# Kernel optimization log

Hardware: AMD Instinct MI355X
Metric: run time of the kernel (lower is better)

The kernel has to match this reference:

```python
import jax, jax.numpy as jnp
import numpy as np

STRIDE = 10  # matches init_kwargs

def setup_inputs() -> dict:
    key = jax.random.key(0)
    x = jax.random.normal(key, (64, 1000, 128), dtype=jnp.float32)
    return {"x": x}

def reference(x):
    B, T, F = x.shape
    L = T // STRIDE  # number of windows
    # (B, L, S, F): non-overlapping windows of length STRIDE
    xr = x.reshape(B, L, STRIDE, F)
    mean = xr.mean(axis=2, keepdims=True)          # avg_pool(ksize=stride, strides=stride)
    ms = xr - mean                                  # means_subtracted
    std = jnp.sqrt(jnp.mean(ms * ms, axis=2))       # (B, L, F), population std
    # per-window covariance: (B, L, F, F)
    cov = jnp.einsum('blsk,blsm->blkm', ms, ms) / STRIDE
    # strictly-lower-triangle indices, row-major order == tf.boolean_mask order
    i, j = np.tril_indices(F, -1)
    cov_v = cov[..., i, j]                          # (B, L, F*(F-1)/2)
    den_v = std[..., i] * std[..., j]               # gather std pairs directly
    safe = jnp.where(den_v == 0, jnp.float32(1.0), den_v)
    return jnp.where(den_v == 0, jnp.float32(0.0), cov_v / safe)  # divide_no_nan
```

## Files before the change

### kernel.cpp

```cpp
#include <hip/hip_runtime.h>

#define BATCH 64
#define TLEN 1000
#define F 128
#define S 10
#define L 100
#define NPAIR 8128
#define NTILE 528
#define NT4 (NPAIR / 4)
#define BLOCK 512

__global__ __launch_bounds__(BLOCK, 8) void corr_kernel(const float* __restrict__ x,
                                                        float* __restrict__ out) {
    const int win = blockIdx.x;
    const int b = win / L;
    const int l = win % L;
    const int tid = threadIdx.x;

    __shared__ float ms[S][F];
    __shared__ __align__(16) float tri[NPAIR];

    const float4* src4 = (const float4*)(x + ((size_t)b * TLEN + (size_t)l * S) * F);
    if (tid < (S * F) / 4) ((float4*)&ms[0][0])[tid] = src4[tid];
    __syncthreads();

    if (tid < F) {
        const int f = tid;
        float col[S];
        float sum = 0.f;
        #pragma unroll
        for (int s = 0; s < S; ++s) { col[s] = ms[s][f]; sum += col[s]; }
        const float mean = sum * (1.0f / S);
        float sq = 0.f;
        #pragma unroll
        for (int s = 0; s < S; ++s) { float d = col[s] - mean; col[s] = d; sq += d * d; }
        const float stdv = sqrtf(sq * (1.0f / S));
        const float r = (stdv == 0.f) ? 0.f : 0.31622776601683794f / stdv;
        #pragma unroll
        for (int s = 0; s < S; ++s) ms[s][f] = col[s] * r;
    }
    __syncthreads();

    for (int t = tid; t < NTILE; t += BLOCK) {
        int ti = (int)((sqrtf(8.0f * (float)t + 1.0f) - 1.0f) * 0.5f);
        while ((ti + 1) * (ti + 2) / 2 <= t) ++ti;
        while (ti * (ti + 1) / 2 > t) --ti;
        const int tj = t - ti * (ti + 1) / 2;

        float acc[4][4];
        #pragma unroll
        for (int a = 0; a < 4; ++a)
            #pragma unroll
            for (int c = 0; c < 4; ++c) acc[a][c] = 0.f;

        #pragma unroll
        for (int s = 0; s < S; ++s) {
            const float4 av = *(const float4*)&ms[s][ti * 4];
            const float4 bv = *(const float4*)&ms[s][tj * 4];
            const float a0[4] = {av.x, av.y, av.z, av.w};
            const float b0[4] = {bv.x, bv.y, bv.z, bv.w};
            #pragma unroll
            for (int di = 0; di < 4; ++di)
                #pragma unroll
                for (int dj = 0; dj < 4; ++dj)
                    acc[di][dj] += a0[di] * b0[dj];
        }

        #pragma unroll
        for (int di = 0; di < 4; ++di) {
            const int i = ti * 4 + di;
            const int rowoff = i * (i - 1) / 2 + tj * 4;
            #pragma unroll
            for (int k = 0; k < 4; ++k) {
                const int dj = (k + tid) & 3;
                const int j = tj * 4 + dj;
                if (j < i) tri[rowoff + dj] = acc[di][dj];
            }
        }
    }
    __syncthreads();

    const float4* t4 = (const float4*)tri;
    float4* o4 = (float4*)(out + (size_t)win * NPAIR);
    for (int p = tid; p < NT4; p += BLOCK) o4[p] = t4[p];
}

extern "C" void kernel_launch(void* const* d_in, const int* in_sizes, int n_in,
                              void* d_out, int out_size, void* d_ws, size_t ws_size,
                              hipStream_t stream) {
    const float* x = (const float*)d_in[0];
    float* out = (float*)d_out;
    corr_kernel<<<BATCH * L, BLOCK, 0, stream>>>(x, out);
}
```

Baseline: 252.4 us.

## Compute raw covariance from global loads and correct with mean/std afterwards

Drops the shared-memory staging of the centered, normalized window. The tile loop now reads raw x directly from global memory (through the cache) and forms E[xy] − mean_i·mean_j, scaled by the inverse stds held in small shared arrays. This removes one barrier and the shared write/read of the normalized data. In exchange it adds repeated global float4 loads per tile and risks cancellation error from the one-pass covariance formula.

```diff
diff --git a/kernel.cpp b/kernel.cpp
--- a/kernel.cpp
+++ b/kernel.cpp
@@ -17,27 +17,25 @@
     const int l = win % L;
     const int tid = threadIdx.x;
 
-    __shared__ float ms[S][F];
+    const float* __restrict__ w = x + ((size_t)b * TLEN + (size_t)l * S) * F;
+
+    __shared__ float mean_s[F];
+    __shared__ float q_s[F];
     __shared__ __align__(16) float tri[NPAIR];
-
-    const float4* src4 = (const float4*)(x + ((size_t)b * TLEN + (size_t)l * S) * F);
-    if (tid < (S * F) / 4) ((float4*)&ms[0][0])[tid] = src4[tid];
-    __syncthreads();
 
     if (tid < F) {
         const int f = tid;
-        float col[S];
+        float v[S];
         float sum = 0.f;
         #pragma unroll
-        for (int s = 0; s < S; ++s) { col[s] = ms[s][f]; sum += col[s]; }
+        for (int s = 0; s < S; ++s) { v[s] = w[s * F + f]; sum += v[s]; }
         const float mean = sum * (1.0f / S);
         float sq = 0.f;
         #pragma unroll
-        for (int s = 0; s < S; ++s) { float d = col[s] - mean; col[s] = d; sq += d * d; }
+        for (int s = 0; s < S; ++s) { const float d = v[s] - mean; sq += d * d; }
         const float stdv = sqrtf(sq * (1.0f / S));
-        const float r = (stdv == 0.f) ? 0.f : 0.31622776601683794f / stdv;
-        #pragma unroll
-        for (int s = 0; s < S; ++s) ms[s][f] = col[s] * r;
+        mean_s[f] = mean;
+        q_s[f] = (stdv == 0.f) ? 0.f : 1.0f / stdv;
     }
     __syncthreads();
 
@@ -55,8 +53,8 @@
 
         #pragma unroll
         for (int s = 0; s < S; ++s) {
-            const float4 av = *(const float4*)&ms[s][ti * 4];
-            const float4 bv = *(const float4*)&ms[s][tj * 4];
+            const float4 av = *(const float4*)(w + s * F + ti * 4);
+            const float4 bv = *(const float4*)(w + s * F + tj * 4);
             const float a0[4] = {av.x, av.y, av.z, av.w};
             const float b0[4] = {bv.x, bv.y, bv.z, bv.w};
             #pragma unroll
@@ -64,6 +62,13 @@
                 #pragma unroll
                 for (int dj = 0; dj < 4; ++dj)
                     acc[di][dj] += a0[di] * b0[dj];
+        }
+
+        float mi[4], mj[4], qi[4], qj[4];
+        #pragma unroll
+        for (int d = 0; d < 4; ++d) {
+            mi[d] = mean_s[ti * 4 + d]; qi[d] = q_s[ti * 4 + d];
+            mj[d] = mean_s[tj * 4 + d]; qj[d] = q_s[tj * 4 + d];
         }
 
         #pragma unroll
@@ -74,7 +79,9 @@
             for (int k = 0; k < 4; ++k) {
                 const int dj = (k + tid) & 3;
                 const int j = tj * 4 + dj;
-                if (j < i) tri[rowoff + dj] = acc[di][dj];
+                if (j < i) {
+                    tri[rowoff + dj] = (acc[di][dj] * (1.0f / S) - mi[di] * mj[dj]) * (qi[di] * qj[dj]);
+                }
             }
         }
     }
```

New measurement: 453.3 us. +79.6%, slower.
